# Kernel tuning notes

Hardware: AMD Instinct MI355X
Metric: run time of the kernel (lower is better)

## Reference

```python
import jax, jax.numpy as jnp
import numpy as np

B = 262144
D = 128          # d_model
DFF = 4 * D      # 512, FFN expansion
T = 16           # num_tiles
TPC = 4          # tiles_per_cluster
NC = T // TPC    # 4 clusters
NOPS = 8         # len(OPCODES)
EMB = 32
FEAT = EMB + 17  # 49
TW, SW, DW = 0.01, 0.005, 0.01  # ternary / sparsity / diversity weights


def ternary_quant(W):
    # per-tile ternary quantization: threshold at 0.7 * mean|W|, scale = mean|W|
    s0 = jnp.mean(jnp.abs(W))
    return s0 * jnp.sign(W) * (jnp.abs(W) > 0.7 * s0).astype(W.dtype)


def setup_inputs() -> dict:
    key = jax.random.key(0)
    ks = jax.random.split(key, 16)
    inp = {
        'op_idx': jax.random.randint(ks[0], (B,), 0, NOPS),
        'a': jax.random.randint(ks[1], (B,), 0, 256),
        'b': jax.random.randint(ks[2], (B,), 0, 256),
        'c': jax.random.randint(ks[3], (B,), 0, 2),
        # parameters
        'op_embed': jax.random.normal(ks[4], (NOPS, EMB), jnp.float32),
        'W_in': jax.random.normal(ks[5], (FEAT, D), jnp.float32) / np.sqrt(FEAT),
        'b_in': jnp.zeros((D,), jnp.float32),
        'Wr': jax.random.normal(ks[6], (D, T), jnp.float32) / np.sqrt(D),
        'W1': jax.random.normal(ks[7], (T, D, DFF), jnp.float32) / np.sqrt(D),
        'W2': jax.random.normal(ks[8], (T, DFF, D), jnp.float32) / np.sqrt(DFF),
        'Wh1': jax.random.normal(ks[9], (D, 64), jnp.float32) / np.sqrt(D),
        'bh1': jnp.zeros((64,), jnp.float32),
        'Wh2': jax.random.normal(ks[10], (64, 8), jnp.float32) / np.sqrt(64),
        'bh2': jnp.zeros((8,), jnp.float32),
    }
    return inp


def reference(op_embed, W_in, b_in, Wr, W1, W2, Wh1, bh1, Wh2, bh2, op_idx, a, b, c):
    bits = lambda v: ((v[:, None] >> jnp.arange(8)) & 1).astype(jnp.float32)  # [B,8]
    emb = op_embed[op_idx]  # [B,32]
    x = jnp.concatenate([emb, bits(a), bits(b), c[:, None].astype(jnp.float32)], axis=1)  # [B,49]
    x = x @ W_in + b_in  # [B,D]

    # tile routing (top-1)
    logits = x @ Wr                      # [B,T]
    probs = jax.nn.softmax(logits, -1)
    idx = jnp.argmax(probs, -1)          # [B]
    gate = jnp.max(probs, -1)            # [B]

    # ternary-quantized per-tile FFN weights
    W1q = jax.vmap(ternary_quant)(W1)    # [T,D,DFF]
    W2q = jax.vmap(ternary_quant)(W2)    # [T,DFF,D]

    out = jnp.zeros_like(x)
    for t in range(T):  # fixed small tile set
        y = jax.nn.gelu(x @ W1q[t]) @ W2q[t]          # [B,D]
        out = out + jnp.where((idx == t)[:, None], y, 0.0)
    out = out * gate[:, None]

    # aux losses
    one_hot = jax.nn.one_hot(idx, T, dtype=x.dtype)
    frac = one_hot.mean(0)               # tokens per tile
    meanp = probs.mean(0)                # mean router prob per tile
    sparsity = T * jnp.sum(frac * meanp)              # load-balance (Switch-style)
    tern = jnp.mean(jnp.abs(W1 - W1q)) + jnp.mean(jnp.abs(W2 - W2q))
    cp = meanp.reshape(NC, TPC).sum(-1)               # cluster usage
    diversity = jnp.sum(cp * jnp.log(cp + 1e-9))      # negative entropy
    aux = TW * tern + SW * sparsity + DW * diversity

    h = jax.nn.relu(out @ Wh1 + bh1)
    result = jax.nn.sigmoid(h @ Wh2 + bh2)  # [B,8]
    return result, idx, aux
```

## Files before the change

kernel.cpp:

```cpp
#include <hip/hip_runtime.h>
#include <hip/hip_bf16.h>
#include <math.h>

typedef __attribute__((ext_vector_type(8))) short short8;
typedef __attribute__((ext_vector_type(4))) float floatx4;
typedef __attribute__((ext_vector_type(4))) unsigned int uintx4;
typedef __attribute__((ext_vector_type(2))) unsigned int uintx2;

__device__ __forceinline__ unsigned short f2bf(float f) {
    unsigned int u = __float_as_uint(f);
    unsigned int r = (u + 0x7fffu + ((u >> 16) & 1u)) >> 16;
    return (unsigned short)r;
}

__device__ __forceinline__ unsigned int cvtpk(float a, float b) {
    unsigned int r;
    asm("v_cvt_pk_bf16_f32 %0, %1, %2" : "=v"(r) : "v"(a), "v"(b));
    return r;
}

__device__ __forceinline__ float gelu_f(float u) {
    float u2 = u * u;
    float p = __builtin_fmaf(u2, -0.102943242f, -2.302208184f);
    float z = p * u;
    float e;
    asm("v_exp_f32 %0, %1" : "=v"(e) : "v"(z));
    return u * __builtin_amdgcn_rcpf(1.0f + e);
}

__device__ __forceinline__ floatx4 mfma16(short8 a, short8 b, floatx4 c) {
    return __builtin_amdgcn_mfma_f32_16x16x32_bf16(a, b, c, 0, 0, 0);
}


__global__ __launch_bounds__(256) void k_sumabs(const float* __restrict__ W1,
                                                const float* __restrict__ W2,
                                                float* __restrict__ partials) {
    int blk = blockIdx.x;
    bool isW1 = blk < 256;
    const float* W = (isW1 ? W1 : W2) + (long)(isW1 ? blk : blk - 256) * 4096;
    float s = 0.f;
    #pragma unroll
    for (int i = 0; i < 4; i++) {
        floatx4 v = *(const floatx4*)(W + i * 1024 + threadIdx.x * 4);
        s += fabsf(v[0]) + fabsf(v[1]) + fabsf(v[2]) + fabsf(v[3]);
    }
    __shared__ float red[256];
    red[threadIdx.x] = s; __syncthreads();
    for (int st = 128; st > 0; st >>= 1) {
        if (threadIdx.x < st) red[threadIdx.x] += red[threadIdx.x + st];
        __syncthreads();
    }
    if (threadIdx.x == 0) partials[blk] = red[0];
}

__global__ __launch_bounds__(256) void k_quant(
        const float* __restrict__ W1, const float* __restrict__ W2,
        const float* __restrict__ partials,
        unsigned short* __restrict__ W1qT, unsigned short* __restrict__ W2qT,
        float* ternsum) {
    int blk = blockIdx.x;
    bool isW1 = blk < 256;
    long el0 = (long)(isW1 ? blk : blk - 256) * 4096;
    int t = (int)(el0 >> 16);
    const float* part = partials + (isW1 ? 0 : 256) + t * 16;
    float ssum = 0.f;
    #pragma unroll
    for (int i = 0; i < 16; i++) ssum += part[i];
    float s = ssum * (1.0f / 65536.0f);
    float thr = 0.7f * s;
    unsigned int us = (unsigned int)f2bf(s);
    const float* Wsrc = (isW1 ? W1 : W2) + el0;
    unsigned short* dst = (isW1 ? W1qT : W2qT) + (long)t * 65536;
    int locbase = (int)(el0 & 65535);
    float dsum = 0.f;
    #pragma unroll
    for (int i = 0; i < 4; i++) {
        int off = i * 1024 + threadIdx.x * 4;
        floatx4 w = *(const floatx4*)(Wsrc + off);
        int loc = locbase + off;
        #pragma unroll
        for (int r = 0; r < 4; r++) {
            float wv = w[r];
            float aw = fabsf(wv);
            bool big = aw > thr;
            dsum += big ? fabsf(aw - s) : aw;
            unsigned int sign15 = (__float_as_uint(wv) >> 16) & 0x8000u;
            unsigned short q = big ? (unsigned short)(us | sign15) : (unsigned short)0;
            int lr = loc + r;
            int addr = isW1 ? ((lr & 511) * 128 + (lr >> 9))
                            : ((lr & 127) * 512 + (lr >> 7));
            dst[addr] = q;
        }
    }
    __shared__ float red[256];
    red[threadIdx.x] = dsum; __syncthreads();
    for (int st2 = 128; st2 > 0; st2 >>= 1) {
        if (threadIdx.x < st2) red[threadIdx.x] += red[threadIdx.x + st2];
        __syncthreads();
    }
    if (threadIdx.x == 0) atomicAdd(ternsum, red[0]);
}

__global__ __launch_bounds__(256) void k_w23(
        const unsigned short* __restrict__ W2qT, const float* __restrict__ Wh1,
        unsigned short* __restrict__ W23qT) {
    int t = blockIdx.x >> 6, h = blockIdx.x & 63;
    __shared__ float wcol[128];
    if (threadIdx.x < 128) wcol[threadIdx.x] = Wh1[threadIdx.x * 64 + h];
    __syncthreads();
    int k2 = threadIdx.x * 2;
    const unsigned short* w2 = W2qT + (long)t * 65536 + k2;
    float a0 = 0.f, a1 = 0.f;
    #pragma unroll 8
    for (int d = 0; d < 128; d++) {
        unsigned int u = *(const unsigned int*)(w2 + d * 512);
        float w = wcol[d];
        a0 += w * __uint_as_float(u << 16);
        a1 += w * __uint_as_float(u & 0xffff0000u);
    }
    *(unsigned int*)(W23qT + ((long)(t * 64 + h)) * 512 + k2) = cvtpk(a0, a1);
}

__global__ void k_tables(const float* __restrict__ op_embed, const float* __restrict__ W_in,
                         const float* __restrict__ b_in,
                         float* embW, float* Ta, float* Tb, float* Tc) {
    int i = blockIdx.x * 256 + threadIdx.x;
    if (i < 1024) {
        int op = i >> 7, j = i & 127;
        float s = b_in[j];
        #pragma unroll
        for (int k = 0; k < 32; k++) s += op_embed[op * 32 + k] * W_in[k * 128 + j];
        embW[i] = s;
    } else if (i < 1024 + 32768) {
        int r = i - 1024; int a = r >> 7, j = r & 127;
        float s = 0.f;
        #pragma unroll
        for (int bit = 0; bit < 8; bit++) if ((a >> bit) & 1) s += W_in[(32 + bit) * 128 + j];
        Ta[r] = s;
    } else if (i < 33792 + 32768) {
        int r = i - 33792; int b = r >> 7, j = r & 127;
        float s = 0.f;
        #pragma unroll
        for (int bit = 0; bit < 8; bit++) if ((b >> bit) & 1) s += W_in[(40 + bit) * 128 + j];
        Tb[r] = s;
    } else if (i < 66560 + 128) {
        int j = i - 66560; Tc[j] = W_in[48 * 128 + j];
    }
}

__global__ void k_tablesR(const float* __restrict__ embW, const float* __restrict__ Ta,
                          const float* __restrict__ Tb, const float* __restrict__ Tc,
                          const float* __restrict__ Wr,
                          float* embWr, float* TaR, float* TbR, float* TcR) {
    int i = blockIdx.x * 256 + threadIdx.x;
    int row = i >> 4, t = i & 15;
    const float* src; float* dst;
    if (row < 8)        { src = embW + row * 128;        dst = embWr + i; }
    else if (row < 264) { src = Ta + (row - 8) * 128;    dst = TaR + (row - 8) * 16 + t; }
    else if (row < 520) { src = Tb + (row - 264) * 128;  dst = TbR + (row - 264) * 16 + t; }
    else if (row == 520){ src = Tc;                      dst = TcR + t; }
    else return;
    float s = 0.f;
    for (int j = 0; j < 128; j++) s += src[j] * Wr[j * 16 + t];
    *dst = s;
}


__global__ __launch_bounds__(256) void k_front(
        const int* __restrict__ op_idx, const int* __restrict__ a_in,
        const int* __restrict__ b_in_i, const int* __restrict__ c_in,
        const float* __restrict__ embW, const float* __restrict__ Ta,
        const float* __restrict__ Tb, const float* __restrict__ Tc,
        const float* __restrict__ embWr, const float* __restrict__ TaR,
        const float* __restrict__ TbR, const float* __restrict__ TcR,
        unsigned short* __restrict__ xq, float* __restrict__ gate_out,
        float* psum, int* cnt, float* __restrict__ d_idx) {
    __shared__ float sp[4][16];
    __shared__ int sc[4][16];
    int gid = blockIdx.x * 256 + threadIdx.x;
    int lane = threadIdx.x & 63;
    int j = lane & 15;
    int grpbase = lane & 48;
    float psum_acc = 0.f; int cnt_acc = 0;

    #pragma unroll 1
    for (int it = 0; it < 16; it++) {
        int tok = it * 16384 + (gid >> 4);
        int op = op_idx[tok], a = a_in[tok], b = b_in_i[tok], c = c_in[tok];
        float cf = (float)c;

        float lg = embWr[op * 16 + j] + TaR[a * 16 + j] + TbR[b * 16 + j] + cf * TcR[j];
        float m = lg;
        m = fmaxf(m, __shfl_xor(m, 8, 16));
        m = fmaxf(m, __shfl_xor(m, 4, 16));
        m = fmaxf(m, __shfl_xor(m, 2, 16));
        m = fmaxf(m, __shfl_xor(m, 1, 16));
        float p = __expf(lg - m);
        float s = p;
        s += __shfl_xor(s, 8, 16);
        s += __shfl_xor(s, 4, 16);
        s += __shfl_xor(s, 2, 16);
        s += __shfl_xor(s, 1, 16);
        float g = __builtin_amdgcn_rcpf(s);
        unsigned long long ball = __ballot(lg == m);
        int bi = __ffsll((unsigned long long)((ball >> grpbase) & 0xffffULL)) - 1;
        psum_acc += p * g;
        cnt_acc += (j == bi) ? 1 : 0;
        if (j == 0) { gate_out[tok] = g; d_idx[tok] = (float)bi; }

        int d0 = j * 8;
        const floatx4* E  = (const floatx4*)(embW + op * 128 + d0);
        const floatx4* A4 = (const floatx4*)(Ta + a * 128 + d0);
        const floatx4* B4 = (const floatx4*)(Tb + b * 128 + d0);
        const floatx4* C4 = (const floatx4*)(Tc + d0);
        floatx4 v0 = E[0] + A4[0] + B4[0] + cf * C4[0];
        floatx4 v1 = E[1] + A4[1] + B4[1] + cf * C4[1];
        uintx4 o;
        o[0] = cvtpk(v0[0], v0[1]);
        o[1] = cvtpk(v0[2], v0[3]);
        o[2] = cvtpk(v1[0], v1[1]);
        o[3] = cvtpk(v1[2], v1[3]);
        *(uintx4*)(xq + (long)tok * 128 + d0) = o;
    }

    psum_acc += __shfl_xor(psum_acc, 16);
    psum_acc += __shfl_xor(psum_acc, 32);
    cnt_acc += __shfl_xor(cnt_acc, 16);
    cnt_acc += __shfl_xor(cnt_acc, 32);
    int wv = threadIdx.x >> 6;
    if (lane < 16) { sp[wv][j] = psum_acc; sc[wv][j] = cnt_acc; }
    __syncthreads();
    if (threadIdx.x < 16) {
        int jj = threadIdx.x;
        atomicAdd(&psum[jj], sp[0][jj] + sp[1][jj] + sp[2][jj] + sp[3][jj]);
        atomicAdd(&cnt[jj], sc[0][jj] + sc[1][jj] + sc[2][jj] + sc[3][jj]);
    }
}


__global__ void k_scatter(const float* __restrict__ d_idx, const int* __restrict__ cnt,
                          int* fill, int* __restrict__ bucket) {
    __shared__ int lc[16], lbase[16];
    if (threadIdx.x < 16) lc[threadIdx.x] = 0;
    __syncthreads();
    int offs[16];
    {
        int off = 0;
        #pragma unroll
        for (int tt = 0; tt < 16; tt++) { offs[tt] = off; off += cnt[tt]; }
    }
    int tok = blockIdx.x * 256 + threadIdx.x;
    int t = (int)d_idx[tok];
    int lpos = atomicAdd(&lc[t], 1);
    __syncthreads();
    if (threadIdx.x < 16) lbase[threadIdx.x] = atomicAdd(&fill[threadIdx.x], lc[threadIdx.x]);
    __syncthreads();
    bucket[offs[t] + lbase[t] + lpos] = tok;
}


__global__ __launch_bounds__(256, 4) void k_ffn(
    const unsigned short* __restrict__ xq, const float* __restrict__ gate,
    const int* __restrict__ bucket, const int* __restrict__ cnt_g,
    const float* __restrict__ psum_g, const float* __restrict__ ternsum_g,
    const unsigned short* __restrict__ W1qT, const unsigned short* __restrict__ W23qT,
    const float* __restrict__ Wh2, const float* __restrict__ bh1,
    const float* __restrict__ bh2,
    float* __restrict__ result, float* __restrict__ d_aux) {

    extern __shared__ __align__(16) unsigned char smem[];
    unsigned short* Ax = (unsigned short*)smem;
    unsigned short* Pb = Ax + 64 * 136;
    int*   toks = (int*)(smem + 34816);
    float* gats = (float*)(smem + 35072);
    float* Wh2l = (float*)(smem + 35328);
    float* bh2l = (float*)(smem + 37376);
    float* bh1l = (float*)(smem + 37408);

    int bid = blockIdx.x;
    int t = -1, ci = 0, nt = 0, base = 0;
    {
        int coff = 0, off = 0;
        #pragma unroll 1
        for (int tt = 0; tt < 16; tt++) {
            int c = cnt_g[tt];
            int ch = (c + 63) >> 6;
            if (t < 0 && bid < coff + ch) { t = tt; ci = bid - coff; nt = c; base = off + ci * 64; }
            coff += ch; off += c;
        }
    }
    if (t < 0) return;
    int nvalid = nt - ci * 64; if (nvalid > 64) nvalid = 64;

    int tid = threadIdx.x;
    if (tid < 64) {
        int tk = (tid < nvalid) ? bucket[base + tid] : -1;
        toks[tid] = tk;
        gats[tid] = (tk >= 0) ? gate[tk] : 0.0f;
    }
    Wh2l[tid] = Wh2[tid];
    Wh2l[tid + 256] = Wh2[tid + 256];
    if (tid < 8) bh2l[tid] = bh2[tid];
    else if (tid < 72) bh1l[tid - 8] = bh1[tid - 8];
    __syncthreads();

    #pragma unroll
    for (int it = 0; it < 4; it++) {
        int seg = it * 256 + tid; int r = seg >> 4, sg = seg & 15;
        int tk = toks[r];
        uintx4 v = {0u, 0u, 0u, 0u};
        if (tk >= 0) v = *(const uintx4*)(xq + (long)tk * 128 + sg * 8);
        *(uintx4*)(Ax + r * 136 + sg * 8) = v;
    }
    __syncthreads();

    int lane = tid & 63, dh = tid >> 6;
    int lane15 = lane & 15, lgrp = lane >> 4;

    floatx4 acc3[4];
    #pragma unroll
    for (int j = 0; j < 4; j++) acc3[j] = (floatx4){0.f, 0.f, 0.f, 0.f};

    const unsigned short* w1p = W1qT + (long)t * 65536 + (dh * 32 + lane15) * 128 + lgrp * 8;
    const unsigned short* w23p = W23qT + ((long)t * 64 + dh * 16 + lane15) * 512 + lgrp * 8;

    for (int nc = 0; nc < 4; nc++) {
        floatx4 acc1[2][4];
        #pragma unroll
        for (int i = 0; i < 2; i++)
            #pragma unroll
            for (int j = 0; j < 4; j++) acc1[i][j] = (floatx4){0.f, 0.f, 0.f, 0.f};

        const unsigned short* w1c = w1p + nc * 16384;
        #pragma unroll
        for (int kk = 0; kk < 4; kk++) {
            short8 af0 = *(const short8*)(w1c + kk * 32);
            short8 af1 = *(const short8*)(w1c + 2048 + kk * 32);
            int ko = kk * 32 + lgrp * 8;
            #pragma unroll
            for (int mt = 0; mt < 4; mt++) {
                short8 bf = *(const short8*)(Ax + (mt * 16 + lane15) * 136 + ko);
                acc1[0][mt] = mfma16(af0, bf, acc1[0][mt]);
                acc1[1][mt] = mfma16(af1, bf, acc1[1][mt]);
            }
        }
        __syncthreads();

        #pragma unroll
        for (int i = 0; i < 2; i++) {
            int k2b = dh * 32 + i * 16 + lgrp * 4;
            #pragma unroll
            for (int mt = 0; mt < 4; mt++) {
                int m = mt * 16 + lane15;
                floatx4 v = acc1[i][mt];
                float g0 = gelu_f(v[0]), g1v = gelu_f(v[1]);
                float g2v = gelu_f(v[2]), g3 = gelu_f(v[3]);
                uintx2 o; o[0] = cvtpk(g0, g1v); o[1] = cvtpk(g2v, g3);
                *(uintx2*)(Pb + m * 136 + k2b) = o;
            }
        }
        __syncthreads();

        const unsigned short* w23c = w23p + nc * 128;
        #pragma unroll
        for (int kk = 0; kk < 4; kk++) {
            short8 af = *(const short8*)(w23c + kk * 32);
            int ko = kk * 32 + lgrp * 8;
            #pragma unroll
            for (int mt = 0; mt < 4; mt++) {
                short8 bf = *(const short8*)(Pb + (mt * 16 + lane15) * 136 + ko);
                acc3[mt] = mfma16(af, bf, acc3[mt]);
            }
        }
    }

    __syncthreads();
    float* H = (float*)Pb;
    int hb = dh * 16 + lgrp * 4;
    floatx4 b4 = *(const floatx4*)(bh1l + hb);
    #pragma unroll
    for (int mt = 0; mt < 4; mt++) {
        int m = mt * 16 + lane15;
        float gm = gats[m];
        floatx4 v;
        v[0] = fmaxf(acc3[mt][0] * gm + b4[0], 0.f);
        v[1] = fmaxf(acc3[mt][1] * gm + b4[1], 0.f);
        v[2] = fmaxf(acc3[mt][2] * gm + b4[2], 0.f);
        v[3] = fmaxf(acc3[mt][3] * gm + b4[3], 0.f);
        *(floatx4*)(H + m * 68 + hb) = v;
    }
    __syncthreads();

    int mloc = tid >> 2, c0 = (tid & 3) * 2;
    int tk = toks[mloc];
    float z0 = bh2l[c0], z1 = bh2l[c0 + 1];
    const floatx4* Hr4 = (const floatx4*)(H + mloc * 68);
    #pragma unroll
    for (int h4 = 0; h4 < 16; h4++) {
        floatx4 hv = Hr4[h4];
        #pragma unroll
        for (int r = 0; r < 4; r++) {
            int h = h4 * 4 + r;
            z0 += hv[r] * Wh2l[h * 8 + c0];
            z1 += hv[r] * Wh2l[h * 8 + c0 + 1];
        }
    }
    if (tk >= 0) {
        float2 rr;
        rr.x = __builtin_amdgcn_rcpf(1.0f + __expf(-z0));
        rr.y = __builtin_amdgcn_rcpf(1.0f + __expf(-z1));
        *(float2*)(result + (long)tk * 8 + c0) = rr;
    }

    if (bid == 0 && tid == 0) {
        const float Bf = 262144.0f;
        float tern = ternsum_g[0] * (1.0f / 1048576.0f);
        float sp = 0.f; float cp[4] = {0.f, 0.f, 0.f, 0.f};
        for (int tt = 0; tt < 16; tt++) {
            float frac = (float)cnt_g[tt] / Bf, mp = psum_g[tt] / Bf;
            sp += frac * mp; cp[tt >> 2] += mp;
        }
        float dv = 0.f;
        for (int cc = 0; cc < 4; cc++) dv += cp[cc] * logf(cp[cc] + 1e-9f);
        d_aux[0] = 0.01f * tern + 0.005f * (16.0f * sp) + 0.01f * dv;
    }
}


extern "C" void kernel_launch(void* const* d_in, const int* in_sizes, int n_in,
                              void* d_out, int out_size, void* d_ws, size_t ws_size,
                              hipStream_t stream) {
    const int* op_idx = (const int*)d_in[0];
    const int* a_in   = (const int*)d_in[1];
    const int* b_in_i = (const int*)d_in[2];
    const int* c_in   = (const int*)d_in[3];
    const float* op_embed = (const float*)d_in[4];
    const float* W_in  = (const float*)d_in[5];
    const float* b_in  = (const float*)d_in[6];
    const float* Wr    = (const float*)d_in[7];
    const float* W1    = (const float*)d_in[8];
    const float* W2    = (const float*)d_in[9];
    const float* Wh1   = (const float*)d_in[10];
    const float* bh1   = (const float*)d_in[11];
    const float* Wh2   = (const float*)d_in[12];
    const float* bh2   = (const float*)d_in[13];

    const long B = in_sizes[0];
    float* result = (float*)d_out;
    float* d_idx  = (float*)d_out + B * 8;
    float* d_aux  = (float*)d_out + B * 9;

    unsigned char* ws = (unsigned char*)d_ws;
    unsigned short* xq    = (unsigned short*)(ws + 0);
    unsigned short* W1qT  = (unsigned short*)(ws + 67108864);
    unsigned short* W2qT  = (unsigned short*)(ws + 69206016);
    unsigned short* W23qT = (unsigned short*)(ws + 71303168);
    float* gate  = (float*)(ws + 72351744);
    int*   bucket= (int*)  (ws + 73400320);
    float* Ta    = (float*)(ws + 74448896);
    float* Tb    = (float*)(ws + 74579968);
    float* embW  = (float*)(ws + 74711040);
    float* Tc    = (float*)(ws + 74715136);
    float* TaR   = (float*)(ws + 74715648);
    float* TbR   = (float*)(ws + 74732032);
    float* embWr = (float*)(ws + 74748416);
    float* TcR   = (float*)(ws + 74748928);
    float* partials = (float*)(ws + 74748992);
    unsigned char* acc = ws + 74751040;
    float* ternsum = (float*)(acc + 0);
    float* psum    = (float*)(acc + 64);
    int*   cnt     = (int*)(acc + 128);
    int*   fill    = (int*)(acc + 192);

    hipMemsetAsync(acc, 0, 256, stream);

    k_sumabs<<<512, 256, 0, stream>>>(W1, W2, partials);
    k_quant<<<512, 256, 0, stream>>>(W1, W2, partials, W1qT, W2qT, ternsum);
    k_tables<<<261, 256, 0, stream>>>(op_embed, W_in, b_in, embW, Ta, Tb, Tc);
    k_tablesR<<<33, 256, 0, stream>>>(embW, Ta, Tb, Tc, Wr, embWr, TaR, TbR, TcR);
    k_front<<<1024, 256, 0, stream>>>(op_idx, a_in, b_in_i, c_in,
                                      embW, Ta, Tb, Tc, embWr, TaR, TbR, TcR,
                                      xq, gate, psum, cnt, d_idx);
    k_w23<<<1024, 256, 0, stream>>>(W2qT, Wh1, W23qT);
    k_scatter<<<(int)(B / 256), 256, 0, stream>>>(d_idx, cnt, fill, bucket);
    k_ffn<<<4112, 256, 37664, stream>>>(xq, gate, bucket, cnt, psum, ternsum,
                                        W1qT, W23qT, Wh2, bh1, bh2, result, d_aux);
}
```

Baseline: 282.1 us.

## Keep GELU intermediate in registers via permlane swaps, split-K second GEMM with LDS reduction

```diff
diff --git a/kernel.cpp b/kernel.cpp
--- a/kernel.cpp
+++ b/kernel.cpp
@@ -17,6 +17,13 @@
     unsigned int r;
     asm("v_cvt_pk_bf16_f32 %0, %1, %2" : "=v"(r) : "v"(a), "v"(b));
     return r;
+}
+
+__device__ __forceinline__ void permlane32_swap(unsigned int &a, unsigned int &b) {
+    asm volatile("v_permlane32_swap_b32 %0, %1" : "+v"(a), "+v"(b));
+}
+__device__ __forceinline__ void permlane16_swap(unsigned int &a, unsigned int &b) {
+    asm volatile("v_permlane16_swap_b32 %0, %1" : "+v"(a), "+v"(b));
 }
 
 __device__ __forceinline__ float gelu_f(float u) {
@@ -260,7 +267,7 @@
 }
 
 
-__global__ __launch_bounds__(256, 4) void k_ffn(
+__global__ __launch_bounds__(256, 3) void k_ffn(
     const unsigned short* __restrict__ xq, const float* __restrict__ gate,
     const int* __restrict__ bucket, const int* __restrict__ cnt_g,
     const float* __restrict__ psum_g, const float* __restrict__ ternsum_g,
@@ -271,12 +278,12 @@
 
     extern __shared__ __align__(16) unsigned char smem[];
     unsigned short* Ax = (unsigned short*)smem;
-    unsigned short* Pb = Ax + 64 * 136;
-    int*   toks = (int*)(smem + 34816);
-    float* gats = (float*)(smem + 35072);
-    float* Wh2l = (float*)(smem + 35328);
-    float* bh2l = (float*)(smem + 37376);
-    float* bh1l = (float*)(smem + 37408);
+    float* Red = (float*)(smem + 17408);
+    int*   toks = (int*)(smem + 50176);
+    float* gats = (float*)(smem + 50432);
+    float* Wh2l = (float*)(smem + 50688);
+    float* bh2l = (float*)(smem + 52736);
+    float* bh1l = (float*)(smem + 52768);
 
     int bid = blockIdx.x;
     int t = -1, ci = 0, nt = 0, base = 0;
@@ -318,12 +325,14 @@
     int lane = tid & 63, dh = tid >> 6;
     int lane15 = lane & 15, lgrp = lane >> 4;
 
-    floatx4 acc3[4];
-    #pragma unroll
-    for (int j = 0; j < 4; j++) acc3[j] = (floatx4){0.f, 0.f, 0.f, 0.f};
-
-    const unsigned short* w1p = W1qT + (long)t * 65536 + (dh * 32 + lane15) * 128 + lgrp * 8;
-    const unsigned short* w23p = W23qT + ((long)t * 64 + dh * 16 + lane15) * 512 + lgrp * 8;
+    floatx4 acc3[4][4];
+    #pragma unroll
+    for (int i = 0; i < 4; i++)
+        #pragma unroll
+        for (int j = 0; j < 4; j++) acc3[i][j] = (floatx4){0.f, 0.f, 0.f, 0.f};
+
+    const unsigned short* w1p  = W1qT + (long)t * 65536 + (dh * 32 + lane15) * 128 + lgrp * 8;
+    const unsigned short* w23p = W23qT + ((long)t * 64 + lane15) * 512 + dh * 32 + lgrp * 8;
 
     for (int nc = 0; nc < 4; nc++) {
         floatx4 acc1[2][4];
@@ -345,38 +354,75 @@
                 acc1[1][mt] = mfma16(af1, bf, acc1[1][mt]);
             }
         }
+
+        const unsigned short* w23c = w23p + nc * 128;
+        short8 af23_0 = *(const short8*)(w23c);
+        short8 af23_1 = *(const short8*)(w23c + 8192);
+        short8 af23_2 = *(const short8*)(w23c + 16384);
+        short8 af23_3 = *(const short8*)(w23c + 24576);
+
+        #pragma unroll
+        for (int mt = 0; mt < 4; mt++) {
+            floatx4 v0 = acc1[0][mt], v1 = acc1[1][mt];
+            unsigned int X0 = cvtpk(gelu_f(v0[0]), gelu_f(v0[1]));
+            unsigned int X1 = cvtpk(gelu_f(v0[2]), gelu_f(v0[3]));
+            unsigned int Y0 = cvtpk(gelu_f(v1[0]), gelu_f(v1[1]));
+            unsigned int Y1 = cvtpk(gelu_f(v1[2]), gelu_f(v1[3]));
+            permlane32_swap(X0, Y0);
+            permlane16_swap(X0, Y0);
+            permlane32_swap(X1, Y1);
+            permlane16_swap(X1, Y1);
+            union { uintx4 u; short8 s; } bu;
+            bu.u[0] = X0; bu.u[1] = X1; bu.u[2] = Y0; bu.u[3] = Y1;
+            short8 bfrag = bu.s;
+            acc3[0][mt] = mfma16(af23_0, bfrag, acc3[0][mt]);
+            acc3[1][mt] = mfma16(af23_1, bfrag, acc3[1][mt]);
+            acc3[2][mt] = mfma16(af23_2, bfrag, acc3[2][mt]);
+            acc3[3][mt] = mfma16(af23_3, bfrag, acc3[3][mt]);
+        }
+    }
+
+    bool hi = (dh & 2) != 0;
+    floatx4 k0[4], k1[4];
+    {
+        float* mybuf = Red + dh * 2048;
+        #pragma unroll
+        for (int mt = 0; mt < 4; mt++) {
+            floatx4 s0 = hi ? acc3[0][mt] : acc3[2][mt];
+            floatx4 s1 = hi ? acc3[1][mt] : acc3[3][mt];
+            *(floatx4*)(mybuf + ((0 * 4 + mt) * 64 + lane) * 4) = s0;
+            *(floatx4*)(mybuf + ((1 * 4 + mt) * 64 + lane) * 4) = s1;
+            k0[mt] = hi ? acc3[2][mt] : acc3[0][mt];
+            k1[mt] = hi ? acc3[3][mt] : acc3[1][mt];
+        }
         __syncthreads();
-
-        #pragma unroll
-        for (int i = 0; i < 2; i++) {
-            int k2b = dh * 32 + i * 16 + lgrp * 4;
-            #pragma unroll
-            for (int mt = 0; mt < 4; mt++) {
-                int m = mt * 16 + lane15;
-                floatx4 v = acc1[i][mt];
-                float g0 = gelu_f(v[0]), g1v = gelu_f(v[1]);
-                float g2v = gelu_f(v[2]), g3 = gelu_f(v[3]);
-                uintx2 o; o[0] = cvtpk(g0, g1v); o[1] = cvtpk(g2v, g3);
-                *(uintx2*)(Pb + m * 136 + k2b) = o;
-            }
+        const float* pbuf = Red + (dh ^ 2) * 2048;
+        #pragma unroll
+        for (int mt = 0; mt < 4; mt++) {
+            k0[mt] += *(const floatx4*)(pbuf + ((0 * 4 + mt) * 64 + lane) * 4);
+            k1[mt] += *(const floatx4*)(pbuf + ((1 * 4 + mt) * 64 + lane) * 4);
+        }
+    }
+    __syncthreads();
+    bool lo1 = (dh & 1) != 0;
+    floatx4 fin[4];
+    {
+        float* mybuf = Red + dh * 1024;
+        #pragma unroll
+        for (int mt = 0; mt < 4; mt++) {
+            floatx4 sm = lo1 ? k0[mt] : k1[mt];
+            *(floatx4*)(mybuf + (mt * 64 + lane) * 4) = sm;
+            fin[mt] = lo1 ? k1[mt] : k0[mt];
         }
         __syncthreads();
-
-        const unsigned short* w23c = w23p + nc * 128;
-        #pragma unroll
-        for (int kk = 0; kk < 4; kk++) {
-            short8 af = *(const short8*)(w23c + kk * 32);
-            int ko = kk * 32 + lgrp * 8;
-            #pragma unroll
-            for (int mt = 0; mt < 4; mt++) {
-                short8 bf = *(const short8*)(Pb + (mt * 16 + lane15) * 136 + ko);
-                acc3[mt] = mfma16(af, bf, acc3[mt]);
-            }
-        }
-    }
-
-    __syncthreads();
-    float* H = (float*)Pb;
+        const float* pbuf = Red + (dh ^ 1) * 1024;
+        #pragma unroll
+        for (int mt = 0; mt < 4; mt++)
+            fin[mt] += *(const floatx4*)(pbuf + (mt * 64 + lane) * 4);
+    }
+    __syncthreads();
+
+    float* H = Red;
     int hb = dh * 16 + lgrp * 4;
     floatx4 b4 = *(const floatx4*)(bh1l + hb);
     #pragma unroll
@@ -384,10 +430,10 @@
         int m = mt * 16 + lane15;
         float gm = gats[m];
         floatx4 v;
-        v[0] = fmaxf(acc3[mt][0] * gm + b4[0], 0.f);
-        v[1] = fmaxf(acc3[mt][1] * gm + b4[1], 0.f);
-        v[2] = fmaxf(acc3[mt][2] * gm + b4[2], 0.f);
-        v[3] = fmaxf(acc3[mt][3] * gm + b4[3], 0.f);
+        v[0] = fmaxf(fin[mt][0] * gm + b4[0], 0.f);
+        v[1] = fmaxf(fin[mt][1] * gm + b4[1], 0.f);
+        v[2] = fmaxf(fin[mt][2] * gm + b4[2], 0.f);
+        v[3] = fmaxf(fin[mt][3] * gm + b4[3], 0.f);
         *(floatx4*)(H + m * 68 + hb) = v;
     }
     __syncthreads();
@@ -484,6 +530,6 @@
                                       xq, gate, psum, cnt, d_idx);
     k_w23<<<1024, 256, 0, stream>>>(W2qT, Wh1, W23qT);
     k_scatter<<<(int)(B / 256), 256, 0, stream>>>(d_idx, cnt, fill, bucket);
-    k_ffn<<<4112, 256, 37664, stream>>>(xq, gate, bucket, cnt, psum, ternsum,
+    k_ffn<<<4112, 256, 53024, stream>>>(xq, gate, bucket, cnt, psum, ternsum,
                                         W1qT, W23qT, Wh2, bh1, bh2, result, d_aux);
 }
```

After: 279.4 us. No clear change (-1.0%).
